# Performance work log

Measured on AMD Instinct MI355X. Metric: run time of the kernel, lower is better.

The kernel has to match this reference:

```python
import jax, jax.numpy as jnp
import numpy as np

EPS = 1e-5
SLOPE = 0.01  # torch LeakyReLU default negative_slope


def _stage(h, W):
    # h: [B, N, k, Cin]; W: [Cout, Cin] (1x1 conv, no bias)
    h = jnp.einsum('bnkc,oc->bnko', h, W)
    # InstanceNorm2d (affine=False): normalize per (batch, channel) over spatial (N, k)
    mean = jnp.mean(h, axis=(1, 2), keepdims=True)
    var = jnp.var(h, axis=(1, 2), keepdims=True)
    h = (h - mean) * jax.lax.rsqrt(var + EPS)
    return jnp.where(h >= 0, h, SLOPE * h)


def setup_inputs() -> dict:
    key = jax.random.key(0)
    k1, k2, k3, k4, k5 = jax.random.split(key, 5)
    B, N, D, K, C = 8, 4096, 64, 20, 64
    x = jax.random.normal(k1, (B, N, D), dtype=jnp.float32)
    ind = jax.random.randint(k2, (B, N, K), 0, B * N, dtype=jnp.int64)
    W1 = jax.random.normal(k3, (C, 2 * D), dtype=jnp.float32) * 0.05
    W2 = jax.random.normal(k4, (C, C), dtype=jnp.float32) * 0.05
    W3 = jax.random.normal(k5, (C, C), dtype=jnp.float32) * 0.05
    return {"x": x, "ind": ind, "W1": W1, "W2": W2, "W3": W3}


def reference(x, ind, W1, W2, W3):
    B, N, D = x.shape
    k = ind.shape[2]
    # Gather neighbors via global (B*N) indices, as in the torch code
    y = x.reshape(B * N, D)[ind.reshape(B * N, k)].reshape(B, N, k, D)  # [B,N,k,D]
    xe = jnp.broadcast_to(x[:, :, None, :], (B, N, k, D))
    feat = jnp.concatenate([y - xe, xe], axis=3)  # [B,N,k,2D]
    h = _stage(feat, W1)
    h = _stage(h, W2)
    h = _stage(h, W3)
    # max-pool over k neighbors -> [B, N, Cout]
    return jnp.max(h, axis=2)
```

## Files before the change

kernel.cpp:

```cpp
#include <hip/hip_runtime.h>

#define BDIM 8
#define NPTS 4096
#define KNEI 20
#define BN (BDIM*NPTS)
#define NKCNT (NPTS*KNEI)
#define EPSI 1e-5f
#define SLOPE 0.01f

typedef _Float16 half_t;
typedef __attribute__((ext_vector_type(2))) _Float16 h2v;
typedef __attribute__((ext_vector_type(4))) _Float16 h4v;
typedef __attribute__((ext_vector_type(8))) _Float16 h8v;
typedef __attribute__((ext_vector_type(4))) float f32x4;
typedef __attribute__((ext_vector_type(2))) float f32x2;

__device__ __forceinline__ h2v cvt2(float a, float b) {
    return __builtin_bit_cast(h2v, __builtin_amdgcn_cvt_pkrtz(a, b));
}
__device__ __forceinline__ unsigned long long pack4_f16(const f32x4& a) {
    unsigned p0 = __builtin_bit_cast(unsigned, cvt2(a[0], a[1]));
    unsigned p1 = __builtin_bit_cast(unsigned, cvt2(a[2], a[3]));
    return ((unsigned long long)p1 << 32) | p0;
}

__global__ __launch_bounds__(256) void k0_uv(const float* __restrict__ x,
        const float* __restrict__ W1, const float* __restrict__ W2,
        const float* __restrict__ W3, half_t* __restrict__ u,
        half_t* __restrict__ v, half_t* __restrict__ Wh2,
        half_t* __restrict__ Wh3) {
    int tid = threadIdx.x;
    if (blockIdx.x >= BN / 64) {
        const float* src = (blockIdx.x == BN / 64) ? W2 : W3;
        half_t* dst = (blockIdx.x == BN / 64) ? Wh2 : Wh3;
        for (int i = tid; i < 4096; i += 256) dst[i] = (half_t)src[i];
        return;
    }
    int lane = tid & 63, w = tid >> 6;
    int l15 = lane & 15, q = lane >> 4;
    int row = blockIdx.x * 64 + w * 16 + l15;
    h8v bx[2];
#pragma unroll
    for (int kc = 0; kc < 2; ++kc) {
        const float* xp = x + (size_t)row * 64 + kc * 32 + q * 8;
        f32x4 x0 = *(const f32x4*)xp;
        f32x4 x1 = *(const f32x4*)(xp + 4);
        h8v t;
#pragma unroll
        for (int j = 0; j < 4; ++j) { t[j] = (half_t)x0[j]; t[4 + j] = (half_t)x1[j]; }
        bx[kc] = t;
    }
    h8v wa[4][2], wd[4][2];
#pragma unroll
    for (int mt = 0; mt < 4; ++mt)
#pragma unroll
        for (int kc = 0; kc < 2; ++kc) {
            const float* wp = W1 + (mt * 16 + l15) * 128 + kc * 32 + q * 8;
            f32x4 a0 = *(const f32x4*)wp;
            f32x4 a1 = *(const f32x4*)(wp + 4);
            f32x4 b0 = *(const f32x4*)(wp + 64);
            f32x4 b1 = *(const f32x4*)(wp + 68);
            h8v ta, td;
#pragma unroll
            for (int j = 0; j < 4; ++j) {
                ta[j] = (half_t)a0[j]; ta[4 + j] = (half_t)a1[j];
                td[j] = (half_t)(b0[j] - a0[j]); td[4 + j] = (half_t)(b1[j] - a1[j]);
            }
            wa[mt][kc] = ta; wd[mt][kc] = td;
        }
#pragma unroll
    for (int mt = 0; mt < 4; ++mt) {
        f32x4 au = {0.f, 0.f, 0.f, 0.f}, av = {0.f, 0.f, 0.f, 0.f};
        au = __builtin_amdgcn_mfma_f32_16x16x32_f16(wa[mt][0], bx[0], au, 0, 0, 0);
        au = __builtin_amdgcn_mfma_f32_16x16x32_f16(wa[mt][1], bx[1], au, 0, 0, 0);
        av = __builtin_amdgcn_mfma_f32_16x16x32_f16(wd[mt][0], bx[0], av, 0, 0, 0);
        av = __builtin_amdgcn_mfma_f32_16x16x32_f16(wd[mt][1], bx[1], av, 0, 0, 0);
        *(unsigned long long*)(u + (size_t)row * 64 + mt * 16 + q * 4) = pack4_f16(au);
        *(unsigned long long*)(v + (size_t)row * 64 + mt * 16 + q * 4) = pack4_f16(av);
    }
}

__global__ __launch_bounds__(256) void k1_stats1(const half_t* __restrict__ u,
        const half_t* __restrict__ v, const int* __restrict__ ind,
        float* __restrict__ s1) {
    __shared__ float sacc[128];
    int tid = threadIdx.x;
    if (tid < 128) sacc[tid] = 0.f;
    int lane = tid & 63, w = tid >> 6;
    int b = blockIdx.x >> 8;
    int n0 = (blockIdx.x & 255) << 4;
    int p = b * NPTS + n0 + w * 4 + (lane >> 4);
    int rh = (lane >> 3) & 1, c8 = lane & 7;
    const int* ip = ind + (size_t)p * 20;
    int idx[10];
#pragma unroll
    for (int r = 0; r < 10; ++r) idx[r] = ip[r * 2 + rh];
    h8v vv = *(const h8v*)(v + (size_t)p * 64 + c8 * 8);
    h8v g[10];
#pragma unroll
    for (int r = 0; r < 10; ++r)
        g[r] = *(const h8v*)(u + (size_t)idx[r] * 64 + c8 * 8);
    float s[8] = {}, qa[8] = {};
#pragma unroll
    for (int r = 0; r < 10; ++r) {
        h8v h = g[r] + vv;
#pragma unroll
        for (int j = 0; j < 8; ++j) {
            float f = (float)h[j];
            s[j] += f; qa[j] = fmaf(f, f, qa[j]);
        }
    }
#pragma unroll
    for (int m = 8; m <= 32; m <<= 1)
#pragma unroll
        for (int j = 0; j < 8; ++j) {
            s[j] += __shfl_xor(s[j], m, 64);
            qa[j] += __shfl_xor(qa[j], m, 64);
        }
    __syncthreads();
    if ((lane & 56) == 0) {
#pragma unroll
        for (int j = 0; j < 8; ++j) {
            atomicAdd(&sacc[c8 * 8 + j], s[j]);
            atomicAdd(&sacc[64 + c8 * 8 + j], qa[j]);
        }
    }
    __syncthreads();
    if (tid < 128)
        atomicAdd(&s1[(tid >> 6) * 512 + b * 64 + (tid & 63)], sacc[tid]);
}

__global__ __launch_bounds__(256, 4) void k2_stats2(const half_t* __restrict__ u,
        const half_t* __restrict__ v, const int* __restrict__ ind,
        const half_t* __restrict__ Wh2, const float* __restrict__ s1,
        float* __restrict__ s2) {
    __shared__ float sacc[128];
    int tid = threadIdx.x;
    if (tid < 128) sacc[tid] = 0.f;
    int lane = tid & 63, w = tid >> 6;
    int l15 = lane & 15, q = lane >> 4;
    int b = blockIdx.x >> 8;
    int n0 = (blockIdx.x & 255) << 4;
    int base = b * NPTS + n0;
    int base20 = base * 20;
    int idxs[5];
#pragma unroll
    for (int nt = 0; nt < 5; ++nt)
        idxs[nt] = ind[base20 + w * 80 + l15 * 5 + nt];
    h8v ug[5][2];
#pragma unroll
    for (int nt = 0; nt < 5; ++nt) {
        const half_t* up = u + (size_t)idxs[nt] * 64 + q * 8;
        ug[nt][0] = *(const h8v*)up;
        ug[nt][1] = *(const h8v*)(up + 32);
    }
    int gp = base + w * 4 + (l15 >> 2);
    h8v vfr[2];
#pragma unroll
    for (int kc = 0; kc < 2; ++kc)
        vfr[kc] = *(const h8v*)(v + (size_t)gp * 64 + kc * 32 + q * 8);
    h8v aw[4][2];
#pragma unroll
    for (int mt = 0; mt < 4; ++mt)
#pragma unroll
        for (int kc = 0; kc < 2; ++kc)
            aw[mt][kc] = *(const h8v*)(Wh2 + (mt * 16 + l15) * 64 + kc * 32 + q * 8);
    const float inv = 1.0f / (float)NKCNT;
    h8v r1v[2], vn[2];
#pragma unroll
    for (int kc = 0; kc < 2; ++kc)
#pragma unroll
        for (int j = 0; j < 8; ++j) {
            int c = kc * 32 + q * 8 + j;
            float mm = s1[b * 64 + c] * inv;
            float va = s1[512 + b * 64 + c] * inv - mm * mm;
            float rs = rsqrtf(va + EPSI);
            r1v[kc][j] = (half_t)rs;
            vn[kc][j] = (half_t)(((float)vfr[kc][j] - mm) * rs);
        }
    float ss[4][4] = {}, sq[4][4] = {};
#pragma unroll
    for (int nt = 0; nt < 5; ++nt) {
        h8v bfr[2];
#pragma unroll
        for (int kc = 0; kc < 2; ++kc) {
            h8v t = ug[nt][kc] * r1v[kc] + vn[kc];
            bfr[kc] = __builtin_elementwise_max(t, t * (half_t)SLOPE);
        }
#pragma unroll
        for (int mt = 0; mt < 4; ++mt) {
            f32x4 a = {0.f, 0.f, 0.f, 0.f};
            a = __builtin_amdgcn_mfma_f32_16x16x32_f16(aw[mt][0], bfr[0], a, 0, 0, 0);
            a = __builtin_amdgcn_mfma_f32_16x16x32_f16(aw[mt][1], bfr[1], a, 0, 0, 0);
#pragma unroll
            for (int j = 0; j < 4; ++j) {
                ss[mt][j] += a[j];
                sq[mt][j] = fmaf(a[j], a[j], sq[mt][j]);
            }
        }
    }
#pragma unroll
    for (int m = 1; m < 16; m <<= 1)
#pragma unroll
        for (int mt = 0; mt < 4; ++mt)
#pragma unroll
            for (int j = 0; j < 4; ++j) {
                ss[mt][j] += __shfl_xor(ss[mt][j], m, 64);
                sq[mt][j] += __shfl_xor(sq[mt][j], m, 64);
            }
    __syncthreads();
    if (l15 == 0) {
#pragma unroll
        for (int mt = 0; mt < 4; ++mt)
#pragma unroll
            for (int j = 0; j < 4; ++j) {
                atomicAdd(&sacc[mt * 16 + q * 4 + j], ss[mt][j]);
                atomicAdd(&sacc[64 + mt * 16 + q * 4 + j], sq[mt][j]);
            }
    }
    __syncthreads();
    if (tid < 128)
        atomicAdd(&s2[(tid >> 6) * 512 + b * 64 + (tid & 63)], sacc[tid]);
}

__global__ __launch_bounds__(256, 4) void k3_fused(const half_t* __restrict__ u,
        const half_t* __restrict__ v, const int* __restrict__ ind,
        const half_t* __restrict__ Wh2, const half_t* __restrict__ Wh3,
        const float* __restrict__ s1, const float* __restrict__ s2,
        float* __restrict__ s3, float* __restrict__ out) {
    __shared__ __align__(16) unsigned char scr[16384];
    __shared__ float sacc[128];
    int tid = threadIdx.x;
    if (tid < 128) sacc[tid] = 0.f;
    int lane = tid & 63, w = tid >> 6;
    int l15 = lane & 15, q = lane >> 4;
    int rw7 = l15 & 7;
    int b = blockIdx.x >> 8;
    int n0 = (blockIdx.x & 255) << 4;
    int base = b * NPTS + n0;
    int base20 = base * 20;
    int idxs[5];
#pragma unroll
    for (int nt = 0; nt < 5; ++nt)
        idxs[nt] = ind[base20 + w * 80 + l15 * 5 + nt];
    const half_t* up0 = u + (size_t)idxs[0] * 64 + q * 8;
    h8v ua = *(const h8v*)up0;
    h8v ub = *(const h8v*)(up0 + 32);
    int gp = base + w * 4 + (l15 >> 2);
    h8v vfr[2];
#pragma unroll
    for (int kc = 0; kc < 2; ++kc)
        vfr[kc] = *(const h8v*)(v + (size_t)gp * 64 + kc * 32 + q * 8);
    h8v aw2[4][2];
#pragma unroll
    for (int mt = 0; mt < 4; ++mt)
#pragma unroll
        for (int kc = 0; kc < 2; ++kc)
            aw2[mt][kc] = *(const h8v*)(Wh2 + (mt * 16 + l15) * 64 + kc * 32 + q * 8);
    const float inv = 1.0f / (float)NKCNT;
    h8v r1v[2], vn[2];
#pragma unroll
    for (int kc = 0; kc < 2; ++kc)
#pragma unroll
        for (int j = 0; j < 8; ++j) {
            int c = kc * 32 + q * 8 + j;
            float mm = s1[b * 64 + c] * inv;
            float va = s1[512 + b * 64 + c] * inv - mm * mm;
            float rs = rsqrtf(va + EPSI);
            r1v[kc][j] = (half_t)rs;
            vn[kc][j] = (half_t)(((float)vfr[kc][j] - mm) * rs);
        }
    unsigned char* scrw0 = scr + w * 4096;
    h8v bf2[5][2];
#pragma unroll
    for (int nt = 0; nt < 5; ++nt) {
        h8v cu0 = ua, cu1 = ub;
        if (nt < 4) {
            const half_t* upn = u + (size_t)idxs[nt + 1] * 64 + q * 8;
            ua = *(const h8v*)upn;
            ub = *(const h8v*)(upn + 32);
        }
        unsigned char* scrw = scrw0 + (nt & 1) * 2048;
        h8v bfr[2];
        {
            h8v t0 = cu0 * r1v[0] + vn[0];
            h8v t1 = cu1 * r1v[1] + vn[1];
            bfr[0] = __builtin_elementwise_max(t0, t0 * (half_t)SLOPE);
            bfr[1] = __builtin_elementwise_max(t1, t1 * (half_t)SLOPE);
        }
#pragma unroll
        for (int mt = 0; mt < 4; ++mt) {
            f32x4 a = {0.f, 0.f, 0.f, 0.f};
            a = __builtin_amdgcn_mfma_f32_16x16x32_f16(aw2[mt][0], bfr[0], a, 0, 0, 0);
            a = __builtin_amdgcn_mfma_f32_16x16x32_f16(aw2[mt][1], bfr[1], a, 0, 0, 0);
            *(unsigned long long*)(scrw + l15 * 128 +
                (((mt * 2 + (q >> 1)) ^ rw7) << 4) + (q & 1) * 8) = pack4_f16(a);
        }
#pragma unroll
        for (int kc = 0; kc < 2; ++kc)
            bf2[nt][kc] = *(const h8v*)(scrw + l15 * 128 + (((kc * 4 + q) ^ rw7) << 4));
    }
    h8v aw3[4][2];
#pragma unroll
    for (int mt = 0; mt < 4; ++mt)
#pragma unroll
        for (int kc = 0; kc < 2; ++kc)
            aw3[mt][kc] = *(const h8v*)(Wh3 + (mt * 16 + l15) * 64 + kc * 32 + q * 8);
    h8v r2v[2], m2v[2];
#pragma unroll
    for (int kc = 0; kc < 2; ++kc)
#pragma unroll
        for (int j = 0; j < 8; ++j) {
            int c = kc * 32 + q * 8 + j;
            float mm2 = s2[b * 64 + c] * inv;
            float va2 = s2[512 + b * 64 + c] * inv - mm2 * mm2;
            float rs2 = rsqrtf(va2 + EPSI);
            r2v[kc][j] = (half_t)rs2;
            m2v[kc][j] = (half_t)(-mm2 * rs2);
        }
    float ss[4][4] = {}, sq[4][4] = {};
    h2v pm[4][2];
#pragma unroll
    for (int mt = 0; mt < 4; ++mt)
#pragma unroll
        for (int r = 0; r < 2; ++r)
            pm[mt][r] = (h2v){(half_t)-65504.f, (half_t)-65504.f};
#pragma unroll
    for (int nt = 0; nt < 5; ++nt) {
        h8v b0, b1;
        {
            h8v t0 = bf2[nt][0] * r2v[0] + m2v[0];
            h8v t1 = bf2[nt][1] * r2v[1] + m2v[1];
            b0 = __builtin_elementwise_max(t0, t0 * (half_t)SLOPE);
            b1 = __builtin_elementwise_max(t1, t1 * (half_t)SLOPE);
        }
#pragma unroll
        for (int mt = 0; mt < 4; ++mt) {
            f32x4 a = {0.f, 0.f, 0.f, 0.f};
            a = __builtin_amdgcn_mfma_f32_16x16x32_f16(aw3[mt][0], b0, a, 0, 0, 0);
            a = __builtin_amdgcn_mfma_f32_16x16x32_f16(aw3[mt][1], b1, a, 0, 0, 0);
#pragma unroll
            for (int j = 0; j < 4; ++j) {
                ss[mt][j] += a[j];
                sq[mt][j] = fmaf(a[j], a[j], sq[mt][j]);
            }
            h2v p0 = cvt2(a[0], a[1]);
            h2v p1 = cvt2(a[2], a[3]);
            pm[mt][0] = __builtin_elementwise_max(pm[mt][0], p0);
            pm[mt][1] = __builtin_elementwise_max(pm[mt][1], p1);
        }
    }
#pragma unroll
    for (int m = 1; m <= 2; m <<= 1)
#pragma unroll
        for (int mt = 0; mt < 4; ++mt)
#pragma unroll
            for (int r = 0; r < 2; ++r) {
                int t = __shfl_xor(__builtin_bit_cast(int, pm[mt][r]), m, 64);
                pm[mt][r] = __builtin_elementwise_max(pm[mt][r],
                               __builtin_bit_cast(h2v, t));
            }
    {
        int ms = l15 & 3;
        h2v sa = ms == 0 ? pm[0][0] : ms == 1 ? pm[1][0] : ms == 2 ? pm[2][0] : pm[3][0];
        h2v sb = ms == 0 ? pm[0][1] : ms == 1 ? pm[1][1] : ms == 2 ? pm[2][1] : pm[3][1];
        f32x4 o = {(float)sa[0], (float)sa[1], (float)sb[0], (float)sb[1]};
        *(f32x4*)(out + (size_t)gp * 64 + ms * 16 + q * 4) = o;
    }
#pragma unroll
    for (int m = 1; m < 16; m <<= 1)
#pragma unroll
        for (int mt = 0; mt < 4; ++mt)
#pragma unroll
            for (int j = 0; j < 4; ++j) {
                ss[mt][j] += __shfl_xor(ss[mt][j], m, 64);
                sq[mt][j] += __shfl_xor(sq[mt][j], m, 64);
            }
    __syncthreads();
    if (l15 == 0) {
#pragma unroll
        for (int mt = 0; mt < 4; ++mt)
#pragma unroll
            for (int j = 0; j < 4; ++j) {
                atomicAdd(&sacc[mt * 16 + q * 4 + j], ss[mt][j]);
                atomicAdd(&sacc[64 + mt * 16 + q * 4 + j], sq[mt][j]);
            }
    }
    __syncthreads();
    if (tid < 128)
        atomicAdd(&s3[(tid >> 6) * 512 + b * 64 + (tid & 63)], sacc[tid]);
}

__global__ __launch_bounds__(256) void k4_final(float* __restrict__ out,
        const float* __restrict__ s3) {
    int idx = blockIdx.x * 256 + threadIdx.x;
    int c = idx & 63;
    int b = idx >> 18;
    const float inv = 1.0f / (float)NKCNT;
    float mm = s3[b * 64 + c] * inv;
    float vv = s3[512 + b * 64 + c] * inv - mm * mm;
    float r = rsqrtf(vv + EPSI);
    float val = (out[idx] - mm) * r;
    out[idx] = val >= 0.f ? val : SLOPE * val;
}

extern "C" void kernel_launch(void* const* d_in, const int* in_sizes, int n_in,
                              void* d_out, int out_size, void* d_ws, size_t ws_size,
                              hipStream_t stream) {
    const float* x   = (const float*)d_in[0];
    const int*   ind = (const int*)d_in[1];
    const float* W1  = (const float*)d_in[2];
    const float* W2  = (const float*)d_in[3];
    const float* W3  = (const float*)d_in[4];
    float* out = (float*)d_out;

    half_t* u   = (half_t*)d_ws;
    half_t* v   = u + (size_t)BN * 64;
    half_t* Wh2 = v + (size_t)BN * 64;
    half_t* Wh3 = Wh2 + 4096;
    float* stats = (float*)(Wh3 + 4096);
    float* s1 = stats;
    float* s2 = stats + 1024;
    float* s3 = stats + 2048;

    (void)hipMemsetAsync(stats, 0, 3 * 1024 * sizeof(float), stream);
    k0_uv<<<dim3(BN / 64 + 2), dim3(256), 0, stream>>>(x, W1, W2, W3, u, v, Wh2, Wh3);
    k1_stats1<<<dim3(BN / 16), dim3(256), 0, stream>>>(u, v, ind, s1);
    k2_stats2<<<dim3(BN / 16), dim3(256), 0, stream>>>(u, v, ind, Wh2, s1, s2);
    k3_fused<<<dim3(BN / 16), dim3(256), 0, stream>>>(u, v, ind, Wh2, Wh3, s1, s2, s3, out);
    k4_final<<<dim3(BN * 64 / 256), dim3(256), 0, stream>>>(out, s3);
}
```

Measured before the change: 192.3 us.

## Stage weights in LDS and software-pipeline stage-2/3 MFMA loops in k3

In k2 the five neighbor gathers are no longer loaded up front; each next gather is prefetched one step ahead, which cuts register pressure. In k3 the Wh2/Wh3 weights are copied into swizzled shared memory instead of being held in registers. The two MFMA stages are interleaved in a single software-pipelined loop, so stage 3 of tile n-1 runs alongside stage 2 of tile n, and the occupancy hint for both kernels is lowered from 4 to 3. The intent is to reduce register pressure and overlap gather latency with compute, at the cost of extra LDS reads, more shared memory per block and a lower occupancy target.

Measured after the change: 180.0 us. -6.4%, faster.

```diff
diff --git a/kernel.cpp b/kernel.cpp
--- a/kernel.cpp
+++ b/kernel.cpp
@@ -130,7 +130,7 @@
         atomicAdd(&s1[(tid >> 6) * 512 + b * 64 + (tid & 63)], sacc[tid]);
 }
 
-__global__ __launch_bounds__(256, 4) void k2_stats2(const half_t* __restrict__ u,
+__global__ __launch_bounds__(256, 3) void k2_stats2(const half_t* __restrict__ u,
         const half_t* __restrict__ v, const int* __restrict__ ind,
         const half_t* __restrict__ Wh2, const float* __restrict__ s1,
         float* __restrict__ s2) {
@@ -147,13 +147,9 @@
 #pragma unroll
     for (int nt = 0; nt < 5; ++nt)
         idxs[nt] = ind[base20 + w * 80 + l15 * 5 + nt];
-    h8v ug[5][2];
-#pragma unroll
-    for (int nt = 0; nt < 5; ++nt) {
-        const half_t* up = u + (size_t)idxs[nt] * 64 + q * 8;
-        ug[nt][0] = *(const h8v*)up;
-        ug[nt][1] = *(const h8v*)(up + 32);
-    }
+    const half_t* up0 = u + (size_t)idxs[0] * 64 + q * 8;
+    h8v cu0 = *(const h8v*)up0;
+    h8v cu1 = *(const h8v*)(up0 + 32);
     int gp = base + w * 4 + (l15 >> 2);
     h8v vfr[2];
 #pragma unroll
@@ -181,23 +177,28 @@
     float ss[4][4] = {}, sq[4][4] = {};
 #pragma unroll
     for (int nt = 0; nt < 5; ++nt) {
-        h8v bfr[2];
-#pragma unroll
-        for (int kc = 0; kc < 2; ++kc) {
-            h8v t = ug[nt][kc] * r1v[kc] + vn[kc];
-            bfr[kc] = __builtin_elementwise_max(t, t * (half_t)SLOPE);
-        }
+        h8v nx0, nx1;
+        if (nt < 4) {
+            const half_t* upn = u + (size_t)idxs[nt + 1] * 64 + q * 8;
+            nx0 = *(const h8v*)upn;
+            nx1 = *(const h8v*)(upn + 32);
+        }
+        h8v t0 = cu0 * r1v[0] + vn[0];
+        h8v t1 = cu1 * r1v[1] + vn[1];
+        h8v b0 = __builtin_elementwise_max(t0, t0 * (half_t)SLOPE);
+        h8v b1 = __builtin_elementwise_max(t1, t1 * (half_t)SLOPE);
 #pragma unroll
         for (int mt = 0; mt < 4; ++mt) {
             f32x4 a = {0.f, 0.f, 0.f, 0.f};
-            a = __builtin_amdgcn_mfma_f32_16x16x32_f16(aw[mt][0], bfr[0], a, 0, 0, 0);
-            a = __builtin_amdgcn_mfma_f32_16x16x32_f16(aw[mt][1], bfr[1], a, 0, 0, 0);
+            a = __builtin_amdgcn_mfma_f32_16x16x32_f16(aw[mt][0], b0, a, 0, 0, 0);
+            a = __builtin_amdgcn_mfma_f32_16x16x32_f16(aw[mt][1], b1, a, 0, 0, 0);
 #pragma unroll
             for (int j = 0; j < 4; ++j) {
                 ss[mt][j] += a[j];
                 sq[mt][j] = fmaf(a[j], a[j], sq[mt][j]);
             }
         }
+        if (nt < 4) { cu0 = nx0; cu1 = nx1; }
     }
 #pragma unroll
     for (int m = 1; m < 16; m <<= 1)
@@ -223,11 +224,12 @@
         atomicAdd(&s2[(tid >> 6) * 512 + b * 64 + (tid & 63)], sacc[tid]);
 }
 
-__global__ __launch_bounds__(256, 4) void k3_fused(const half_t* __restrict__ u,
+__global__ __launch_bounds__(256, 3) void k3_fused(const half_t* __restrict__ u,
         const half_t* __restrict__ v, const int* __restrict__ ind,
         const half_t* __restrict__ Wh2, const half_t* __restrict__ Wh3,
         const float* __restrict__ s1, const float* __restrict__ s2,
         float* __restrict__ s3, float* __restrict__ out) {
+    __shared__ __align__(16) unsigned char wlds[16384];
     __shared__ __align__(16) unsigned char scr[16384];
     __shared__ float sacc[128];
     int tid = threadIdx.x;
@@ -239,26 +241,27 @@
     int n0 = (blockIdx.x & 255) << 4;
     int base = b * NPTS + n0;
     int base20 = base * 20;
+    for (int i = tid; i < 512; i += 256) {
+        int rw = i >> 3, ch = i & 7;
+        *(h8v*)(wlds + rw * 128 + ((ch ^ (rw & 7)) << 4)) =
+            *(const h8v*)(Wh2 + rw * 64 + ch * 8);
+        *(h8v*)(wlds + 8192 + rw * 128 + ((ch ^ (rw & 7)) << 4)) =
+            *(const h8v*)(Wh3 + rw * 64 + ch * 8);
+    }
     int idxs[5];
 #pragma unroll
     for (int nt = 0; nt < 5; ++nt)
         idxs[nt] = ind[base20 + w * 80 + l15 * 5 + nt];
     const half_t* up0 = u + (size_t)idxs[0] * 64 + q * 8;
-    h8v ua = *(const h8v*)up0;
-    h8v ub = *(const h8v*)(up0 + 32);
+    h8v cu0 = *(const h8v*)up0;
+    h8v cu1 = *(const h8v*)(up0 + 32);
     int gp = base + w * 4 + (l15 >> 2);
     h8v vfr[2];
 #pragma unroll
     for (int kc = 0; kc < 2; ++kc)
         vfr[kc] = *(const h8v*)(v + (size_t)gp * 64 + kc * 32 + q * 8);
-    h8v aw2[4][2];
-#pragma unroll
-    for (int mt = 0; mt < 4; ++mt)
-#pragma unroll
-        for (int kc = 0; kc < 2; ++kc)
-            aw2[mt][kc] = *(const h8v*)(Wh2 + (mt * 16 + l15) * 64 + kc * 32 + q * 8);
     const float inv = 1.0f / (float)NKCNT;
-    h8v r1v[2], vn[2];
+    h8v r1v[2], vn[2], r2v[2], m2v[2];
 #pragma unroll
     for (int kc = 0; kc < 2; ++kc)
 #pragma unroll
@@ -269,55 +272,14 @@
             float rs = rsqrtf(va + EPSI);
             r1v[kc][j] = (half_t)rs;
             vn[kc][j] = (half_t)(((float)vfr[kc][j] - mm) * rs);
-        }
-    unsigned char* scrw0 = scr + w * 4096;
-    h8v bf2[5][2];
-#pragma unroll
-    for (int nt = 0; nt < 5; ++nt) {
-        h8v cu0 = ua, cu1 = ub;
-        if (nt < 4) {
-            const half_t* upn = u + (size_t)idxs[nt + 1] * 64 + q * 8;
-            ua = *(const h8v*)upn;
-            ub = *(const h8v*)(upn + 32);
-        }
-        unsigned char* scrw = scrw0 + (nt & 1) * 2048;
-        h8v bfr[2];
-        {
-            h8v t0 = cu0 * r1v[0] + vn[0];
-            h8v t1 = cu1 * r1v[1] + vn[1];
-            bfr[0] = __builtin_elementwise_max(t0, t0 * (half_t)SLOPE);
-            bfr[1] = __builtin_elementwise_max(t1, t1 * (half_t)SLOPE);
-        }
-#pragma unroll
-        for (int mt = 0; mt < 4; ++mt) {
-            f32x4 a = {0.f, 0.f, 0.f, 0.f};
-            a = __builtin_amdgcn_mfma_f32_16x16x32_f16(aw2[mt][0], bfr[0], a, 0, 0, 0);
-            a = __builtin_amdgcn_mfma_f32_16x16x32_f16(aw2[mt][1], bfr[1], a, 0, 0, 0);
-            *(unsigned long long*)(scrw + l15 * 128 +
-                (((mt * 2 + (q >> 1)) ^ rw7) << 4) + (q & 1) * 8) = pack4_f16(a);
-        }
-#pragma unroll
-        for (int kc = 0; kc < 2; ++kc)
-            bf2[nt][kc] = *(const h8v*)(scrw + l15 * 128 + (((kc * 4 + q) ^ rw7) << 4));
-    }
-    h8v aw3[4][2];
-#pragma unroll
-    for (int mt = 0; mt < 4; ++mt)
-#pragma unroll
-        for (int kc = 0; kc < 2; ++kc)
-            aw3[mt][kc] = *(const h8v*)(Wh3 + (mt * 16 + l15) * 64 + kc * 32 + q * 8);
-    h8v r2v[2], m2v[2];
-#pragma unroll
-    for (int kc = 0; kc < 2; ++kc)
-#pragma unroll
-        for (int j = 0; j < 8; ++j) {
-            int c = kc * 32 + q * 8 + j;
             float mm2 = s2[b * 64 + c] * inv;
             float va2 = s2[512 + b * 64 + c] * inv - mm2 * mm2;
             float rs2 = rsqrtf(va2 + EPSI);
             r2v[kc][j] = (half_t)rs2;
             m2v[kc][j] = (half_t)(-mm2 * rs2);
         }
+    unsigned char* scrw0 = scr + w * 4096;
+    __syncthreads();
     float ss[4][4] = {}, sq[4][4] = {};
     h2v pm[4][2];
 #pragma unroll
@@ -326,28 +288,57 @@
         for (int r = 0; r < 2; ++r)
             pm[mt][r] = (h2v){(half_t)-65504.f, (half_t)-65504.f};
 #pragma unroll
-    for (int nt = 0; nt < 5; ++nt) {
-        h8v b0, b1;
-        {
-            h8v t0 = bf2[nt][0] * r2v[0] + m2v[0];
-            h8v t1 = bf2[nt][1] * r2v[1] + m2v[1];
-            b0 = __builtin_elementwise_max(t0, t0 * (half_t)SLOPE);
-            b1 = __builtin_elementwise_max(t1, t1 * (half_t)SLOPE);
-        }
-#pragma unroll
-        for (int mt = 0; mt < 4; ++mt) {
-            f32x4 a = {0.f, 0.f, 0.f, 0.f};
-            a = __builtin_amdgcn_mfma_f32_16x16x32_f16(aw3[mt][0], b0, a, 0, 0, 0);
-            a = __builtin_amdgcn_mfma_f32_16x16x32_f16(aw3[mt][1], b1, a, 0, 0, 0);
-#pragma unroll
-            for (int j = 0; j < 4; ++j) {
-                ss[mt][j] += a[j];
-                sq[mt][j] = fmaf(a[j], a[j], sq[mt][j]);
-            }
-            h2v p0 = cvt2(a[0], a[1]);
-            h2v p1 = cvt2(a[2], a[3]);
-            pm[mt][0] = __builtin_elementwise_max(pm[mt][0], p0);
-            pm[mt][1] = __builtin_elementwise_max(pm[mt][1], p1);
+    for (int nt = 0; nt < 6; ++nt) {
+        if (nt < 5) {
+            h8v nx0, nx1;
+            if (nt < 4) {
+                const half_t* upn = u + (size_t)idxs[nt + 1] * 64 + q * 8;
+                nx0 = *(const h8v*)upn;
+                nx1 = *(const h8v*)(upn + 32);
+            }
+            unsigned char* scrw = scrw0 + (nt & 1) * 2048;
+            h8v t0 = cu0 * r1v[0] + vn[0];
+            h8v t1 = cu1 * r1v[1] + vn[1];
+            h8v b0 = __builtin_elementwise_max(t0, t0 * (half_t)SLOPE);
+            h8v b1 = __builtin_elementwise_max(t1, t1 * (half_t)SLOPE);
+#pragma unroll
+            for (int mt = 0; mt < 4; ++mt) {
+                h8v w0 = *(const h8v*)(wlds + (mt * 16 + l15) * 128 + ((q ^ rw7) << 4));
+                h8v w1 = *(const h8v*)(wlds + (mt * 16 + l15) * 128 + (((4 + q) ^ rw7) << 4));
+                f32x4 a = {0.f, 0.f, 0.f, 0.f};
+                a = __builtin_amdgcn_mfma_f32_16x16x32_f16(w0, b0, a, 0, 0, 0);
+                a = __builtin_amdgcn_mfma_f32_16x16x32_f16(w1, b1, a, 0, 0, 0);
+                *(unsigned long long*)(scrw + l15 * 128 +
+                    (((mt * 2 + (q >> 1)) ^ rw7) << 4) + (q & 1) * 8) = pack4_f16(a);
+            }
+            if (nt < 4) { cu0 = nx0; cu1 = nx1; }
+        }
+        if (nt > 0) {
+            int m = nt - 1;
+            unsigned char* scrr = scrw0 + (m & 1) * 2048;
+            h8v hr0 = *(const h8v*)(scrr + l15 * 128 + ((q ^ rw7) << 4));
+            h8v hr1 = *(const h8v*)(scrr + l15 * 128 + (((4 + q) ^ rw7) << 4));
+            h8v t0 = hr0 * r2v[0] + m2v[0];
+            h8v t1 = hr1 * r2v[1] + m2v[1];
+            h8v b0 = __builtin_elementwise_max(t0, t0 * (half_t)SLOPE);
+            h8v b1 = __builtin_elementwise_max(t1, t1 * (half_t)SLOPE);
+#pragma unroll
+            for (int mt = 0; mt < 4; ++mt) {
+                h8v w0 = *(const h8v*)(wlds + 8192 + (mt * 16 + l15) * 128 + ((q ^ rw7) << 4));
+                h8v w1 = *(const h8v*)(wlds + 8192 + (mt * 16 + l15) * 128 + (((4 + q) ^ rw7) << 4));
+                f32x4 a = {0.f, 0.f, 0.f, 0.f};
+                a = __builtin_amdgcn_mfma_f32_16x16x32_f16(w0, b0, a, 0, 0, 0);
+                a = __builtin_amdgcn_mfma_f32_16x16x32_f16(w1, b1, a, 0, 0, 0);
+#pragma unroll
+                for (int j = 0; j < 4; ++j) {
+                    ss[mt][j] += a[j];
+                    sq[mt][j] = fmaf(a[j], a[j], sq[mt][j]);
+                }
+                h2v p0 = cvt2(a[0], a[1]);
+                h2v p1 = cvt2(a[2], a[3]);
+                pm[mt][0] = __builtin_elementwise_max(pm[mt][0], p0);
+                pm[mt][1] = __builtin_elementwise_max(pm[mt][1], p1);
+            }
         }
     }
 #pragma unroll
@@ -376,7 +367,6 @@
                 ss[mt][j] += __shfl_xor(ss[mt][j], m, 64);
                 sq[mt][j] += __shfl_xor(sq[mt][j], m, 64);
             }
-    __syncthreads();
     if (l15 == 0) {
 #pragma unroll
         for (int mt = 0; mt < 4; ++mt)
```
